# Kernel optimization log

Measured on AMD Instinct MI355X. Metric: run time of the kernel, lower is better.

## Reference

```python
import jax, jax.numpy as jnp
import numpy as np

B = 2_000_000
CLAMP_MIN = 0.01
NORM_EPS = 1e-5


def setup_inputs() -> dict:
    key = jax.random.key(0)
    F = jax.random.normal(key, (B, 3, 3), dtype=jnp.float32)
    # learned scalar parameters (per init_kwargs)
    youngs_modulus_log = jnp.asarray(13.0, dtype=jnp.float32)
    poissons_ratio = jnp.asarray(0.3, dtype=jnp.float32)
    yield_stress = jnp.asarray(3000.0, dtype=jnp.float32)
    return {
        "F": F,
        "youngs_modulus_log": youngs_modulus_log,
        "poissons_ratio": poissons_ratio,
        "yield_stress": yield_stress,
    }


def reference(F, youngs_modulus_log, poissons_ratio, yield_stress):
    # von-Mises return mapping on singular values of the deformation gradient
    youngs_modulus = jnp.exp(youngs_modulus_log)
    mu = youngs_modulus / (2.0 * (1.0 + poissons_ratio))  # shear modulus

    # batched 3x3 SVD: U (B,3,3), sigma (B,3), Vh (B,3,3)
    U, sigma, Vh = jnp.linalg.svd(F, full_matrices=False)

    sigma = jnp.maximum(sigma, CLAMP_MIN)
    epsilon = jnp.log(sigma)                                  # (B,3) Hencky strain
    epsilon_trace = jnp.sum(epsilon, axis=1, keepdims=True)   # (B,1)
    epsilon_bar = epsilon - epsilon_trace / 3.0               # deviatoric strain
    epsilon_bar_norm = jnp.linalg.norm(epsilon_bar, axis=1, keepdims=True) + NORM_EPS

    delta_gamma = epsilon_bar_norm - yield_stress / (2.0 * mu)  # (B,1)
    yield_epsilon = epsilon - (delta_gamma / epsilon_bar_norm) * epsilon_bar
    yield_sigma = jnp.exp(yield_epsilon)

    sigma = jnp.where(delta_gamma > 0.0, yield_sigma, sigma)  # (B,3)

    # F_corrected = U @ diag(sigma) @ Vh, fused without materializing diag
    F_corrected = jnp.einsum("bij,bj,bjk->bik", U, sigma, Vh)
    return F_corrected
```

## Files before the change

### kernel.cpp

```cpp
#include <hip/hip_runtime.h>
#include <math.h>

#define TPB 256
#define MPB (TPB * 2)

typedef float v2  __attribute__((ext_vector_type(2)));
typedef int   v2i __attribute__((ext_vector_type(2)));

static __device__ __forceinline__ v2 V2(float x){ v2 r; r.x = x; r.y = x; return r; }
static __device__ __forceinline__ v2 vfma(v2 a, v2 b, v2 c){ return __builtin_elementwise_fma(a, b, c); }
static __device__ __forceinline__ v2 vmax(v2 a, v2 b){ return __builtin_elementwise_max(a, b); }
static __device__ __forceinline__ v2 vabs(v2 a){ return __builtin_elementwise_abs(a); }
static __device__ __forceinline__ v2 vcps(v2 a, v2 b){ return __builtin_elementwise_copysign(a, b); }

static __device__ __forceinline__ v2 rsq2(v2 x){ v2 r; r.x = __builtin_amdgcn_rsqf(x.x);  r.y = __builtin_amdgcn_rsqf(x.y);  return r; }
static __device__ __forceinline__ v2 rcp2(v2 x){ v2 r; r.x = __builtin_amdgcn_rcpf(x.x);  r.y = __builtin_amdgcn_rcpf(x.y);  return r; }
static __device__ __forceinline__ v2 sqt2(v2 x){ v2 r; r.x = __builtin_amdgcn_sqrtf(x.x); r.y = __builtin_amdgcn_sqrtf(x.y); return r; }
static __device__ __forceinline__ v2 lg22(v2 x){ v2 r; r.x = __builtin_amdgcn_logf(x.x);  r.y = __builtin_amdgcn_logf(x.y);  return r; }
static __device__ __forceinline__ v2 ex22(v2 x){ v2 r; r.x = __builtin_amdgcn_exp2f(x.x); r.y = __builtin_amdgcn_exp2f(x.y); return r; }

static __device__ __forceinline__ v2 vsel(v2i m, v2 a, v2 b){
  v2i ai = __builtin_bit_cast(v2i, a), bi = __builtin_bit_cast(v2i, b);
  return __builtin_bit_cast(v2, (ai & m) | (bi & ~m));
}

__device__ __forceinline__ void jcs2(v2 app_in, v2 aqq_in, v2 apq,
                                     v2& c, v2& s,
                                     v2& app_out, v2& aqq_out)
{
  v2 d    = (aqq_in - app_in) * 0.5f;
  v2 r2   = vmax(vfma(d, d, apq * apq), V2(1e-60f));
  v2 invh = rsq2(r2);
  v2 h    = r2 * invh;
  v2 sg   = vcps(V2(1.0f), d);
  v2 ch   = h + vabs(d);
  v2 sh   = apq * sg;
  v2 w    = rsq2(vfma(ch, ch, sh * sh));
  c = ch * w;
  s = sh * w;
  v2 hs = h * sg;
  v2 m  = app_in + d;
  app_out = m - hs;
  aqq_out = m + hs;
}

__device__ __forceinline__ void jrot(v2& app, v2& aqq, v2& apq,
                                     v2& apk, v2& aqk,
                                     v2& vp0, v2& vp1, v2& vp2,
                                     v2& vq0, v2& vq1, v2& vq2)
{
  v2 c, s;
  jcs2(app, aqq, apq, c, s, app, aqq);
  apq = V2(0.0f);
  v2 pk = apk, qk = aqk;
  apk = c * pk - s * qk;
  aqk = s * pk + c * qk;
  v2 v;
  v = vp0; vp0 = c*v - s*vq0; vq0 = s*v + c*vq0;
  v = vp1; vp1 = c*v - s*vq1; vq1 = s*v + c*vq1;
  v = vp2; vp2 = c*v - s*vq2; vq2 = s*v + c*vq2;
}

#define CSWAP(li, lj, a0, a1, a2, b0, b1, b2)                                   \
  do {                                                                          \
    v2i _m = (li) < (lj);                                                       \
    v2 _t;                                                                      \
    _t = vsel(_m,(lj),(li)); (lj) = vsel(_m,(li),(lj)); (li) = _t;              \
    _t = vsel(_m,(b0),(a0)); (b0) = vsel(_m,(a0),(b0)); (a0) = _t;              \
    _t = vsel(_m,(b1),(a1)); (b1) = vsel(_m,(a1),(b1)); (a1) = _t;              \
    _t = vsel(_m,(b2),(a2)); (b2) = vsel(_m,(a2),(b2)); (a2) = _t;              \
  } while (0)

__global__ __launch_bounds__(TPB) void plastic_svd_kernel(
    const float* __restrict__ F,
    const float* __restrict__ p_yml,
    const float* __restrict__ p_nu,
    const float* __restrict__ p_ys,
    float* __restrict__ out,
    int nmat)
{
  __shared__ float lds[MPB * 9];
  const int tid = threadIdx.x;
  const int blockBase = blockIdx.x * MPB;
  const int gbase = blockBase * 9;
  const int rem = nmat - blockBase;
  const int nfl = (rem >= MPB ? MPB : rem) * 9;
  const int nfl4 = nfl >> 2;

  {
    const float4* g4 = (const float4*)(F + gbase);
    float4* l4 = (float4*)lds;
    #pragma unroll
    for (int k = 0; k < 5; ++k) {
      int i4 = k * TPB + tid;
      if (i4 < nfl4) l4[i4] = g4[i4];
    }
    int i = (nfl & ~3) + tid;
    if (i < nfl) lds[i] = F[gbase + i];
    for (int i2 = nfl + tid; i2 < MPB * 9; i2 += TPB) lds[i2] = 0.0f;
  }
  __syncthreads();

  const int mi0 = blockBase + tid;
  const int mi1 = blockBase + TPB + tid;
  const float* mA = &lds[tid * 9];
  const float* mB = &lds[(tid + TPB) * 9];
  v2 f00,f01,f02,f10,f11,f12,f20,f21,f22;
  f00.x=mA[0]; f01.x=mA[1]; f02.x=mA[2];
  f10.x=mA[3]; f11.x=mA[4]; f12.x=mA[5];
  f20.x=mA[6]; f21.x=mA[7]; f22.x=mA[8];
  f00.y=mB[0]; f01.y=mB[1]; f02.y=mB[2];
  f10.y=mB[3]; f11.y=mB[4]; f12.y=mB[5];
  f20.y=mB[6]; f21.y=mB[7]; f22.y=mB[8];

  const float mu_s = __builtin_amdgcn_exp2f(p_yml[0] * 1.44269504f) *
                     __builtin_amdgcn_rcpf(2.0f * (1.0f + p_nu[0]));
  const float qy_s = p_ys[0] * 0.5f * __builtin_amdgcn_rcpf(mu_s);
  const v2 qy = V2(qy_s);

  v2 s00 = f00*f00 + f10*f10 + f20*f20;
  v2 s11 = f01*f01 + f11*f11 + f21*f21;
  v2 s22 = f02*f02 + f12*f12 + f22*f22;
  v2 s01 = f00*f01 + f10*f11 + f20*f21;
  v2 s02 = f00*f02 + f10*f12 + f20*f22;
  v2 s12 = f01*f02 + f11*f12 + f21*f22;

  v2 v00,v01,v02,v10,v11,v12,v20,v21,v22;
  v2 c, s;

  jcs2(s00, s11, s01, c, s, s00, s11);
  { v2 pk = s02, qk = s12; s02 = c*pk - s*qk; s12 = s*pk + c*qk; }
  v00 = c;  v01 = s;
  v10 = -s; v11 = c;
  s01 = V2(0.0f);
  jcs2(s00, s22, s02, c, s, s00, s22);
  { v2 pk = s01, qk = s12; s01 = c*pk - s*qk; s12 = s*pk + c*qk; }
  v02 = s * v00; v12 = s * v10; v22 = c;
  v00 = c * v00; v10 = c * v10; v20 = -s;
  v21 = V2(0.0f);
  s02 = V2(0.0f);
  jrot(s11, s22, s12, s01, s02, v01, v11, v21, v02, v12, v22);
  jrot(s00, s11, s01, s02, s12, v00, v10, v20, v01, v11, v21);
  jrot(s00, s22, s02, s01, s12, v00, v10, v20, v02, v12, v22);
  jrot(s11, s22, s12, s01, s02, v01, v11, v21, v02, v12, v22);
  jrot(s00, s11, s01, s02, s12, v00, v10, v20, v01, v11, v21);
  jrot(s00, s22, s02, s01, s12, v00, v10, v20, v02, v12, v22);
  jcs2(s11, s22, s12, c, s, s11, s22);
  { v2 v;
    v = v01; v01 = c*v - s*v02; v02 = s*v + c*v02;
    v = v11; v11 = c*v - s*v12; v12 = s*v + c*v12;
    v = v21; v21 = c*v - s*v22; v22 = s*v + c*v22; }

  v2 l0 = s00, l1 = s11, l2 = s22;
  CSWAP(l0, l1, v00, v10, v20, v01, v11, v21);
  CSWAP(l1, l2, v01, v11, v21, v02, v12, v22);
  CSWAP(l0, l1, v00, v10, v20, v01, v11, v21);

  v2 w0x = f00*v00 + f01*v10 + f02*v20;
  v2 w0y = f10*v00 + f11*v10 + f12*v20;
  v2 w0z = f20*v00 + f21*v10 + f22*v20;
  v2 n0sq = w0x*w0x + w0y*w0y + w0z*w0z;
  v2 inv0 = rsq2(vmax(n0sq, V2(1e-40f)));
  v2 sig0 = n0sq * inv0;
  v2 u0x = w0x*inv0, u0y = w0y*inv0, u0z = w0z*inv0;

  v2 w1x = f00*v01 + f01*v11 + f02*v21;
  v2 w1y = f10*v01 + f11*v11 + f12*v21;
  v2 w1z = f20*v01 + f21*v11 + f22*v21;
  v2 sig1 = sqt2(w1x*w1x + w1y*w1y + w1z*w1z);
  v2 d01 = w1x*u0x + w1y*u0y + w1z*u0z;
  w1x = w1x - d01*u0x; w1y = w1y - d01*u0y; w1z = w1z - d01*u0z;
  v2 n1sq = w1x*w1x + w1y*w1y + w1z*w1z;
  v2 inv1 = rsq2(vmax(n1sq, V2(1e-40f)));
  v2 u1x = w1x*inv1, u1y = w1y*inv1, u1z = w1z*inv1;

  v2 u2x = u0y*u1z - u0z*u1y;
  v2 u2y = u0z*u1x - u0x*u1z;
  v2 u2z = u0x*u1y - u0y*u1x;
  v2 w2x = f00*v02 + f01*v12 + f02*v22;
  v2 w2y = f10*v02 + f11*v12 + f12*v22;
  v2 w2z = f20*v02 + f21*v12 + f22*v22;
  v2 s2d = u2x*w2x + u2y*w2y + u2z*w2z;
  v2i _neg = s2d < V2(0.0f);
  v2 sg = vsel(_neg, V2(-1.0f), V2(1.0f));
  v2 sig2 = s2d * sg;
  u2x = u2x * sg; u2y = u2y * sg; u2z = u2z * sg;

  v2 c0 = vmax(sig0, V2(0.01f));
  v2 c1 = vmax(sig1, V2(0.01f));
  v2 c2 = vmax(sig2, V2(0.01f));
  v2 e0 = lg22(c0), e1 = lg22(c1), e2 = lg22(c2);
  v2 m3 = (e0 + e1 + e2) * (1.0f / 3.0f);
  v2 b0 = e0 - m3, b1 = e1 - m3, b2 = e2 - m3;
  v2 bn = sqt2(b0*b0 + b1*b1 + b2*b2) * 0.69314718f + V2(1e-5f);
  v2 r = vmax(bn - qy, V2(0.0f)) * rcp2(bn);
  c0 = ex22(e0 - r * b0);
  c1 = ex22(e1 - r * b1);
  c2 = ex22(e2 - r * b2);

  v2 a0x = c0*u0x, a0y = c0*u0y, a0z = c0*u0z;
  v2 a1x = c1*u1x, a1y = c1*u1y, a1z = c1*u1z;
  v2 a2x = c2*u2x, a2y = c2*u2y, a2z = c2*u2z;

  v2 o00 = a0x*v00 + a1x*v01 + a2x*v02;
  v2 o01 = a0x*v10 + a1x*v11 + a2x*v12;
  v2 o02 = a0x*v20 + a1x*v21 + a2x*v22;
  v2 o10 = a0y*v00 + a1y*v01 + a2y*v02;
  v2 o11 = a0y*v10 + a1y*v11 + a2y*v12;
  v2 o12 = a0y*v20 + a1y*v21 + a2y*v22;
  v2 o20 = a0z*v00 + a1z*v01 + a2z*v02;
  v2 o21 = a0z*v10 + a1z*v11 + a2z*v12;
  v2 o22 = a0z*v20 + a1z*v21 + a2z*v22;

  if (mi0 < nmat) {
    float* m = &lds[tid * 9];
    m[0]=o00.x; m[1]=o01.x; m[2]=o02.x;
    m[3]=o10.x; m[4]=o11.x; m[5]=o12.x;
    m[6]=o20.x; m[7]=o21.x; m[8]=o22.x;
  }
  if (mi1 < nmat) {
    float* m = &lds[(tid + TPB) * 9];
    m[0]=o00.y; m[1]=o01.y; m[2]=o02.y;
    m[3]=o10.y; m[4]=o11.y; m[5]=o12.y;
    m[6]=o20.y; m[7]=o21.y; m[8]=o22.y;
  }
  __syncthreads();

  {
    float4* g4 = (float4*)(out + gbase);
    const float4* l4 = (const float4*)lds;
    #pragma unroll
    for (int k = 0; k < 5; ++k) {
      int i4 = k * TPB + tid;
      if (i4 < nfl4) g4[i4] = l4[i4];
    }
    int i = (nfl & ~3) + tid;
    if (i < nfl) out[gbase + i] = lds[i];
  }
}

extern "C" void kernel_launch(void* const* d_in, const int* in_sizes, int n_in,
                              void* d_out, int out_size, void* d_ws, size_t ws_size,
                              hipStream_t stream) {
  const float* F     = (const float*)d_in[0];
  const float* p_yml = (const float*)d_in[1];
  const float* p_nu  = (const float*)d_in[2];
  const float* p_ys  = (const float*)d_in[3];
  float* out = (float*)d_out;

  const int nmat = in_sizes[0] / 9;
  const int nblocks = (nmat + MPB - 1) / MPB;
  hipLaunchKernelGGL(plastic_svd_kernel, dim3(nblocks), dim3(TPB), 0, stream,
                     F, p_yml, p_nu, p_ys, out, nmat);
}
```

Before: 33.18 us.

## Process four matrices per thread with v4 vectors and reload F from LDS

```diff
diff --git a/kernel.cpp b/kernel.cpp
--- a/kernel.cpp
+++ b/kernel.cpp
@@ -2,60 +2,71 @@
 #include <math.h>
 
 #define TPB 256
-#define MPB (TPB * 2)
-
-typedef float v2  __attribute__((ext_vector_type(2)));
-typedef int   v2i __attribute__((ext_vector_type(2)));
-
-static __device__ __forceinline__ v2 V2(float x){ v2 r; r.x = x; r.y = x; return r; }
-static __device__ __forceinline__ v2 vfma(v2 a, v2 b, v2 c){ return __builtin_elementwise_fma(a, b, c); }
-static __device__ __forceinline__ v2 vmax(v2 a, v2 b){ return __builtin_elementwise_max(a, b); }
-static __device__ __forceinline__ v2 vabs(v2 a){ return __builtin_elementwise_abs(a); }
-static __device__ __forceinline__ v2 vcps(v2 a, v2 b){ return __builtin_elementwise_copysign(a, b); }
-
-static __device__ __forceinline__ v2 rsq2(v2 x){ v2 r; r.x = __builtin_amdgcn_rsqf(x.x);  r.y = __builtin_amdgcn_rsqf(x.y);  return r; }
-static __device__ __forceinline__ v2 rcp2(v2 x){ v2 r; r.x = __builtin_amdgcn_rcpf(x.x);  r.y = __builtin_amdgcn_rcpf(x.y);  return r; }
-static __device__ __forceinline__ v2 sqt2(v2 x){ v2 r; r.x = __builtin_amdgcn_sqrtf(x.x); r.y = __builtin_amdgcn_sqrtf(x.y); return r; }
-static __device__ __forceinline__ v2 lg22(v2 x){ v2 r; r.x = __builtin_amdgcn_logf(x.x);  r.y = __builtin_amdgcn_logf(x.y);  return r; }
-static __device__ __forceinline__ v2 ex22(v2 x){ v2 r; r.x = __builtin_amdgcn_exp2f(x.x); r.y = __builtin_amdgcn_exp2f(x.y); return r; }
-
-static __device__ __forceinline__ v2 vsel(v2i m, v2 a, v2 b){
-  v2i ai = __builtin_bit_cast(v2i, a), bi = __builtin_bit_cast(v2i, b);
-  return __builtin_bit_cast(v2, (ai & m) | (bi & ~m));
-}
-
-__device__ __forceinline__ void jcs2(v2 app_in, v2 aqq_in, v2 apq,
-                                     v2& c, v2& s,
-                                     v2& app_out, v2& aqq_out)
+#define NQ 4
+#define MPB (TPB * NQ)
+
+typedef float v4  __attribute__((ext_vector_type(4)));
+typedef int   v4i __attribute__((ext_vector_type(4)));
+
+static __device__ __forceinline__ v4 V4(float x){ v4 r; r.x=x; r.y=x; r.z=x; r.w=x; return r; }
+static __device__ __forceinline__ v4 vfma(v4 a, v4 b, v4 c){ return __builtin_elementwise_fma(a, b, c); }
+static __device__ __forceinline__ v4 vmax(v4 a, v4 b){ return __builtin_elementwise_max(a, b); }
+static __device__ __forceinline__ v4 vabs(v4 a){ return __builtin_elementwise_abs(a); }
+static __device__ __forceinline__ v4 vcps(v4 a, v4 b){ return __builtin_elementwise_copysign(a, b); }
+
+static __device__ __forceinline__ v4 rsq4(v4 x){
+  v4 r; r.x=__builtin_amdgcn_rsqf(x.x); r.y=__builtin_amdgcn_rsqf(x.y);
+        r.z=__builtin_amdgcn_rsqf(x.z); r.w=__builtin_amdgcn_rsqf(x.w); return r; }
+static __device__ __forceinline__ v4 rcp4(v4 x){
+  v4 r; r.x=__builtin_amdgcn_rcpf(x.x); r.y=__builtin_amdgcn_rcpf(x.y);
+        r.z=__builtin_amdgcn_rcpf(x.z); r.w=__builtin_amdgcn_rcpf(x.w); return r; }
+static __device__ __forceinline__ v4 sqt4(v4 x){
+  v4 r; r.x=__builtin_amdgcn_sqrtf(x.x); r.y=__builtin_amdgcn_sqrtf(x.y);
+        r.z=__builtin_amdgcn_sqrtf(x.z); r.w=__builtin_amdgcn_sqrtf(x.w); return r; }
+static __device__ __forceinline__ v4 lg24(v4 x){
+  v4 r; r.x=__builtin_amdgcn_logf(x.x); r.y=__builtin_amdgcn_logf(x.y);
+        r.z=__builtin_amdgcn_logf(x.z); r.w=__builtin_amdgcn_logf(x.w); return r; }
+static __device__ __forceinline__ v4 ex24(v4 x){
+  v4 r; r.x=__builtin_amdgcn_exp2f(x.x); r.y=__builtin_amdgcn_exp2f(x.y);
+        r.z=__builtin_amdgcn_exp2f(x.z); r.w=__builtin_amdgcn_exp2f(x.w); return r; }
+
+static __device__ __forceinline__ v4 vsel(v4i m, v4 a, v4 b){
+  v4i ai = __builtin_bit_cast(v4i, a), bi = __builtin_bit_cast(v4i, b);
+  return __builtin_bit_cast(v4, (ai & m) | (bi & ~m));
+}
+
+__device__ __forceinline__ void jcs2(v4 app_in, v4 aqq_in, v4 apq,
+                                     v4& c, v4& s,
+                                     v4& app_out, v4& aqq_out)
 {
-  v2 d    = (aqq_in - app_in) * 0.5f;
-  v2 r2   = vmax(vfma(d, d, apq * apq), V2(1e-60f));
-  v2 invh = rsq2(r2);
-  v2 h    = r2 * invh;
-  v2 sg   = vcps(V2(1.0f), d);
-  v2 ch   = h + vabs(d);
-  v2 sh   = apq * sg;
-  v2 w    = rsq2(vfma(ch, ch, sh * sh));
+  v4 d    = (aqq_in - app_in) * 0.5f;
+  v4 r2   = vmax(vfma(d, d, apq * apq), V4(1e-30f));
+  v4 invh = rsq4(r2);
+  v4 h    = r2 * invh;
+  v4 sg   = vcps(V4(1.0f), d);
+  v4 ch   = h + vabs(d);
+  v4 sh   = apq * sg;
+  v4 w    = rsq4(vfma(ch, ch, sh * sh));
   c = ch * w;
   s = sh * w;
-  v2 hs = h * sg;
-  v2 m  = app_in + d;
+  v4 hs = h * sg;
+  v4 m  = app_in + d;
   app_out = m - hs;
   aqq_out = m + hs;
 }
 
-__device__ __forceinline__ void jrot(v2& app, v2& aqq, v2& apq,
-                                     v2& apk, v2& aqk,
-                                     v2& vp0, v2& vp1, v2& vp2,
-                                     v2& vq0, v2& vq1, v2& vq2)
+__device__ __forceinline__ void jrot(v4& app, v4& aqq, v4& apq,
+                                     v4& apk, v4& aqk,
+                                     v4& vp0, v4& vp1, v4& vp2,
+                                     v4& vq0, v4& vq1, v4& vq2)
 {
-  v2 c, s;
+  v4 c, s;
   jcs2(app, aqq, apq, c, s, app, aqq);
-  apq = V2(0.0f);
-  v2 pk = apk, qk = aqk;
+  apq = V4(0.0f);
+  v4 pk = apk, qk = aqk;
   apk = c * pk - s * qk;
   aqk = s * pk + c * qk;
-  v2 v;
+  v4 v;
   v = vp0; vp0 = c*v - s*vq0; vq0 = s*v + c*vq0;
   v = vp1; vp1 = c*v - s*vq1; vq1 = s*v + c*vq1;
   v = vp2; vp2 = c*v - s*vq2; vq2 = s*v + c*vq2;
@@ -63,8 +74,8 @@
 
 #define CSWAP(li, lj, a0, a1, a2, b0, b1, b2)                                   \
   do {                                                                          \
-    v2i _m = (li) < (lj);                                                       \
-    v2 _t;                                                                      \
+    v4i _m = (li) < (lj);                                                       \
+    v4 _t;                                                                      \
     _t = vsel(_m,(lj),(li)); (lj) = vsel(_m,(li),(lj)); (li) = _t;              \
     _t = vsel(_m,(b0),(a0)); (b0) = vsel(_m,(a0),(b0)); (a0) = _t;              \
     _t = vsel(_m,(b1),(a1)); (b1) = vsel(_m,(a1),(b1)); (a1) = _t;              \
@@ -91,7 +102,7 @@
     const float4* g4 = (const float4*)(F + gbase);
     float4* l4 = (float4*)lds;
     #pragma unroll
-    for (int k = 0; k < 5; ++k) {
+    for (int k = 0; k < 9; ++k) {
       int i4 = k * TPB + tid;
       if (i4 < nfl4) l4[i4] = g4[i4];
     }
@@ -101,44 +112,44 @@
   }
   __syncthreads();
 
-  const int mi0 = blockBase + tid;
-  const int mi1 = blockBase + TPB + tid;
-  const float* mA = &lds[tid * 9];
-  const float* mB = &lds[(tid + TPB) * 9];
-  v2 f00,f01,f02,f10,f11,f12,f20,f21,f22;
-  f00.x=mA[0]; f01.x=mA[1]; f02.x=mA[2];
-  f10.x=mA[3]; f11.x=mA[4]; f12.x=mA[5];
-  f20.x=mA[6]; f21.x=mA[7]; f22.x=mA[8];
-  f00.y=mB[0]; f01.y=mB[1]; f02.y=mB[2];
-  f10.y=mB[3]; f11.y=mB[4]; f12.y=mB[5];
-  f20.y=mB[6]; f21.y=mB[7]; f22.y=mB[8];
+
+  v4 s00, s11, s22, s01, s02, s12;
+  {
+    v4 f00,f01,f02,f10,f11,f12,f20,f21,f22;
+    #pragma unroll
+    for (int q = 0; q < NQ; ++q) {
+      const float* m = &lds[(q * TPB + tid) * 9];
+      f00[q]=m[0]; f01[q]=m[1]; f02[q]=m[2];
+      f10[q]=m[3]; f11[q]=m[4]; f12[q]=m[5];
+      f20[q]=m[6]; f21[q]=m[7]; f22[q]=m[8];
+    }
+    s00 = f00*f00 + f10*f10 + f20*f20;
+    s11 = f01*f01 + f11*f11 + f21*f21;
+    s22 = f02*f02 + f12*f12 + f22*f22;
+    s01 = f00*f01 + f10*f11 + f20*f21;
+    s02 = f00*f02 + f10*f12 + f20*f22;
+    s12 = f01*f02 + f11*f12 + f21*f22;
+  }
 
   const float mu_s = __builtin_amdgcn_exp2f(p_yml[0] * 1.44269504f) *
                      __builtin_amdgcn_rcpf(2.0f * (1.0f + p_nu[0]));
   const float qy_s = p_ys[0] * 0.5f * __builtin_amdgcn_rcpf(mu_s);
-  const v2 qy = V2(qy_s);
-
-  v2 s00 = f00*f00 + f10*f10 + f20*f20;
-  v2 s11 = f01*f01 + f11*f11 + f21*f21;
-  v2 s22 = f02*f02 + f12*f12 + f22*f22;
-  v2 s01 = f00*f01 + f10*f11 + f20*f21;
-  v2 s02 = f00*f02 + f10*f12 + f20*f22;
-  v2 s12 = f01*f02 + f11*f12 + f21*f22;
-
-  v2 v00,v01,v02,v10,v11,v12,v20,v21,v22;
-  v2 c, s;
+  const v4 qy = V4(qy_s);
+
+  v4 v00,v01,v02,v10,v11,v12,v20,v21,v22;
+  v4 c, s;
 
   jcs2(s00, s11, s01, c, s, s00, s11);
-  { v2 pk = s02, qk = s12; s02 = c*pk - s*qk; s12 = s*pk + c*qk; }
+  { v4 pk = s02, qk = s12; s02 = c*pk - s*qk; s12 = s*pk + c*qk; }
   v00 = c;  v01 = s;
   v10 = -s; v11 = c;
-  s01 = V2(0.0f);
+  s01 = V4(0.0f);
   jcs2(s00, s22, s02, c, s, s00, s22);
-  { v2 pk = s01, qk = s12; s01 = c*pk - s*qk; s12 = s*pk + c*qk; }
+  { v4 pk = s01, qk = s12; s01 = c*pk - s*qk; s12 = s*pk + c*qk; }
   v02 = s * v00; v12 = s * v10; v22 = c;
   v00 = c * v00; v10 = c * v10; v20 = -s;
-  v21 = V2(0.0f);
-  s02 = V2(0.0f);
+  v21 = V4(0.0f);
+  s02 = V4(0.0f);
   jrot(s11, s22, s12, s01, s02, v01, v11, v21, v02, v12, v22);
   jrot(s00, s11, s01, s02, s12, v00, v10, v20, v01, v11, v21);
   jrot(s00, s22, s02, s01, s12, v00, v10, v20, v02, v12, v22);
@@ -146,83 +157,89 @@
   jrot(s00, s11, s01, s02, s12, v00, v10, v20, v01, v11, v21);
   jrot(s00, s22, s02, s01, s12, v00, v10, v20, v02, v12, v22);
   jcs2(s11, s22, s12, c, s, s11, s22);
-  { v2 v;
+  { v4 v;
     v = v01; v01 = c*v - s*v02; v02 = s*v + c*v02;
     v = v11; v11 = c*v - s*v12; v12 = s*v + c*v12;
     v = v21; v21 = c*v - s*v22; v22 = s*v + c*v22; }
 
-  v2 l0 = s00, l1 = s11, l2 = s22;
+  v4 l0 = s00, l1 = s11, l2 = s22;
   CSWAP(l0, l1, v00, v10, v20, v01, v11, v21);
   CSWAP(l1, l2, v01, v11, v21, v02, v12, v22);
   CSWAP(l0, l1, v00, v10, v20, v01, v11, v21);
 
-  v2 w0x = f00*v00 + f01*v10 + f02*v20;
-  v2 w0y = f10*v00 + f11*v10 + f12*v20;
-  v2 w0z = f20*v00 + f21*v10 + f22*v20;
-  v2 n0sq = w0x*w0x + w0y*w0y + w0z*w0z;
-  v2 inv0 = rsq2(vmax(n0sq, V2(1e-40f)));
-  v2 sig0 = n0sq * inv0;
-  v2 u0x = w0x*inv0, u0y = w0y*inv0, u0z = w0z*inv0;
-
-  v2 w1x = f00*v01 + f01*v11 + f02*v21;
-  v2 w1y = f10*v01 + f11*v11 + f12*v21;
-  v2 w1z = f20*v01 + f21*v11 + f22*v21;
-  v2 sig1 = sqt2(w1x*w1x + w1y*w1y + w1z*w1z);
-  v2 d01 = w1x*u0x + w1y*u0y + w1z*u0z;
+  v4 f00,f01,f02,f10,f11,f12,f20,f21,f22;
+  #pragma unroll
+  for (int q = 0; q < NQ; ++q) {
+    const float* m = &lds[(q * TPB + tid) * 9];
+    f00[q]=m[0]; f01[q]=m[1]; f02[q]=m[2];
+    f10[q]=m[3]; f11[q]=m[4]; f12[q]=m[5];
+    f20[q]=m[6]; f21[q]=m[7]; f22[q]=m[8];
+  }
+
+  v4 w0x = f00*v00 + f01*v10 + f02*v20;
+  v4 w0y = f10*v00 + f11*v10 + f12*v20;
+  v4 w0z = f20*v00 + f21*v10 + f22*v20;
+  v4 n0sq = w0x*w0x + w0y*w0y + w0z*w0z;
+  v4 inv0 = rsq4(vmax(n0sq, V4(1e-30f)));
+  v4 sig0 = n0sq * inv0;
+  v4 u0x = w0x*inv0, u0y = w0y*inv0, u0z = w0z*inv0;
+
+  v4 w1x = f00*v01 + f01*v11 + f02*v21;
+  v4 w1y = f10*v01 + f11*v11 + f12*v21;
+  v4 w1z = f20*v01 + f21*v11 + f22*v21;
+  v4 sig1 = sqt4(w1x*w1x + w1y*w1y + w1z*w1z);
+  v4 d01 = w1x*u0x + w1y*u0y + w1z*u0z;
   w1x = w1x - d01*u0x; w1y = w1y - d01*u0y; w1z = w1z - d01*u0z;
-  v2 n1sq = w1x*w1x + w1y*w1y + w1z*w1z;
-  v2 inv1 = rsq2(vmax(n1sq, V2(1e-40f)));
-  v2 u1x = w1x*inv1, u1y = w1y*inv1, u1z = w1z*inv1;
-
-  v2 u2x = u0y*u1z - u0z*u1y;
-  v2 u2y = u0z*u1x - u0x*u1z;
-  v2 u2z = u0x*u1y - u0y*u1x;
-  v2 w2x = f00*v02 + f01*v12 + f02*v22;
-  v2 w2y = f10*v02 + f11*v12 + f12*v22;
-  v2 w2z = f20*v02 + f21*v12 + f22*v22;
-  v2 s2d = u2x*w2x + u2y*w2y + u2z*w2z;
-  v2i _neg = s2d < V2(0.0f);
-  v2 sg = vsel(_neg, V2(-1.0f), V2(1.0f));
-  v2 sig2 = s2d * sg;
+  v4 n1sq = w1x*w1x + w1y*w1y + w1z*w1z;
+  v4 inv1 = rsq4(vmax(n1sq, V4(1e-30f)));
+  v4 u1x = w1x*inv1, u1y = w1y*inv1, u1z = w1z*inv1;
+
+  v4 u2x = u0y*u1z - u0z*u1y;
+  v4 u2y = u0z*u1x - u0x*u1z;
+  v4 u2z = u0x*u1y - u0y*u1x;
+  v4 w2x = f00*v02 + f01*v12 + f02*v22;
+  v4 w2y = f10*v02 + f11*v12 + f12*v22;
+  v4 w2z = f20*v02 + f21*v12 + f22*v22;
+  v4 s2d = u2x*w2x + u2y*w2y + u2z*w2z;
+  v4i _neg = s2d < V4(0.0f);
+  v4 sg = vsel(_neg, V4(-1.0f), V4(1.0f));
+  v4 sig2 = s2d * sg;
   u2x = u2x * sg; u2y = u2y * sg; u2z = u2z * sg;
 
-  v2 c0 = vmax(sig0, V2(0.01f));
-  v2 c1 = vmax(sig1, V2(0.01f));
-  v2 c2 = vmax(sig2, V2(0.01f));
-  v2 e0 = lg22(c0), e1 = lg22(c1), e2 = lg22(c2);
-  v2 m3 = (e0 + e1 + e2) * (1.0f / 3.0f);
-  v2 b0 = e0 - m3, b1 = e1 - m3, b2 = e2 - m3;
-  v2 bn = sqt2(b0*b0 + b1*b1 + b2*b2) * 0.69314718f + V2(1e-5f);
-  v2 r = vmax(bn - qy, V2(0.0f)) * rcp2(bn);
-  c0 = ex22(e0 - r * b0);
-  c1 = ex22(e1 - r * b1);
-  c2 = ex22(e2 - r * b2);
-
-  v2 a0x = c0*u0x, a0y = c0*u0y, a0z = c0*u0z;
-  v2 a1x = c1*u1x, a1y = c1*u1y, a1z = c1*u1z;
-  v2 a2x = c2*u2x, a2y = c2*u2y, a2z = c2*u2z;
-
-  v2 o00 = a0x*v00 + a1x*v01 + a2x*v02;
-  v2 o01 = a0x*v10 + a1x*v11 + a2x*v12;
-  v2 o02 = a0x*v20 + a1x*v21 + a2x*v22;
-  v2 o10 = a0y*v00 + a1y*v01 + a2y*v02;
-  v2 o11 = a0y*v10 + a1y*v11 + a2y*v12;
-  v2 o12 = a0y*v20 + a1y*v21 + a2y*v22;
-  v2 o20 = a0z*v00 + a1z*v01 + a2z*v02;
-  v2 o21 = a0z*v10 + a1z*v11 + a2z*v12;
-  v2 o22 = a0z*v20 + a1z*v21 + a2z*v22;
-
-  if (mi0 < nmat) {
-    float* m = &lds[tid * 9];
-    m[0]=o00.x; m[1]=o01.x; m[2]=o02.x;
-    m[3]=o10.x; m[4]=o11.x; m[5]=o12.x;
-    m[6]=o20.x; m[7]=o21.x; m[8]=o22.x;
-  }
-  if (mi1 < nmat) {
-    float* m = &lds[(tid + TPB) * 9];
-    m[0]=o00.y; m[1]=o01.y; m[2]=o02.y;
-    m[3]=o10.y; m[4]=o11.y; m[5]=o12.y;
-    m[6]=o20.y; m[7]=o21.y; m[8]=o22.y;
+  v4 c0 = vmax(sig0, V4(0.01f));
+  v4 c1 = vmax(sig1, V4(0.01f));
+  v4 c2 = vmax(sig2, V4(0.01f));
+  v4 e0 = lg24(c0), e1 = lg24(c1), e2 = lg24(c2);
+  v4 m3 = (e0 + e1 + e2) * (1.0f / 3.0f);
+  v4 b0 = e0 - m3, b1 = e1 - m3, b2 = e2 - m3;
+  v4 bn = sqt4(b0*b0 + b1*b1 + b2*b2) * 0.69314718f + V4(1e-5f);
+  v4 r = vmax(bn - qy, V4(0.0f)) * rcp4(bn);
+  c0 = ex24(e0 - r * b0);
+  c1 = ex24(e1 - r * b1);
+  c2 = ex24(e2 - r * b2);
+
+  v4 a0x = c0*u0x, a0y = c0*u0y, a0z = c0*u0z;
+  v4 a1x = c1*u1x, a1y = c1*u1y, a1z = c1*u1z;
+  v4 a2x = c2*u2x, a2y = c2*u2y, a2z = c2*u2z;
+
+  v4 o00 = a0x*v00 + a1x*v01 + a2x*v02;
+  v4 o01 = a0x*v10 + a1x*v11 + a2x*v12;
+  v4 o02 = a0x*v20 + a1x*v21 + a2x*v22;
+  v4 o10 = a0y*v00 + a1y*v01 + a2y*v02;
+  v4 o11 = a0y*v10 + a1y*v11 + a2y*v12;
+  v4 o12 = a0y*v20 + a1y*v21 + a2y*v22;
+  v4 o20 = a0z*v00 + a1z*v01 + a2z*v02;
+  v4 o21 = a0z*v10 + a1z*v11 + a2z*v12;
+  v4 o22 = a0z*v20 + a1z*v21 + a2z*v22;
+
+  #pragma unroll
+  for (int q = 0; q < NQ; ++q) {
+    if (blockBase + q * TPB + tid < nmat) {
+      float* m = &lds[(q * TPB + tid) * 9];
+      m[0]=o00[q]; m[1]=o01[q]; m[2]=o02[q];
+      m[3]=o10[q]; m[4]=o11[q]; m[5]=o12[q];
+      m[6]=o20[q]; m[7]=o21[q]; m[8]=o22[q];
+    }
   }
   __syncthreads();
 
@@ -230,7 +247,7 @@
     float4* g4 = (float4*)(out + gbase);
     const float4* l4 = (const float4*)lds;
     #pragma unroll
-    for (int k = 0; k < 5; ++k) {
+    for (int k = 0; k < 9; ++k) {
       int i4 = k * TPB + tid;
       if (i4 < nfl4) g4[i4] = l4[i4];
     }
```

New measurement: 36.47 us. 9.9% more time.

## Use persistent blocks with double-buffered async global-to-LDS loads and direct stores

Applied to the files above, without the earlier changes.

```diff
diff --git a/kernel.cpp b/kernel.cpp
--- a/kernel.cpp
+++ b/kernel.cpp
@@ -2,26 +2,36 @@
 #include <math.h>
 
 #define TPB 256
-#define MPB (TPB * 2)
+#define NQ 2
+#define CHUNK (TPB * NQ)
+#define CH_F (CHUNK * 9)
+#define CH_F4 (CH_F / 4)
 
 typedef float v2  __attribute__((ext_vector_type(2)));
 typedef int   v2i __attribute__((ext_vector_type(2)));
-
-static __device__ __forceinline__ v2 V2(float x){ v2 r; r.x = x; r.y = x; return r; }
+typedef float f4u __attribute__((ext_vector_type(4), aligned(4)));
+
+static __device__ __forceinline__ v2 V2(float x){ v2 r; r.x=x; r.y=x; return r; }
 static __device__ __forceinline__ v2 vfma(v2 a, v2 b, v2 c){ return __builtin_elementwise_fma(a, b, c); }
 static __device__ __forceinline__ v2 vmax(v2 a, v2 b){ return __builtin_elementwise_max(a, b); }
 static __device__ __forceinline__ v2 vabs(v2 a){ return __builtin_elementwise_abs(a); }
 static __device__ __forceinline__ v2 vcps(v2 a, v2 b){ return __builtin_elementwise_copysign(a, b); }
 
-static __device__ __forceinline__ v2 rsq2(v2 x){ v2 r; r.x = __builtin_amdgcn_rsqf(x.x);  r.y = __builtin_amdgcn_rsqf(x.y);  return r; }
-static __device__ __forceinline__ v2 rcp2(v2 x){ v2 r; r.x = __builtin_amdgcn_rcpf(x.x);  r.y = __builtin_amdgcn_rcpf(x.y);  return r; }
-static __device__ __forceinline__ v2 sqt2(v2 x){ v2 r; r.x = __builtin_amdgcn_sqrtf(x.x); r.y = __builtin_amdgcn_sqrtf(x.y); return r; }
-static __device__ __forceinline__ v2 lg22(v2 x){ v2 r; r.x = __builtin_amdgcn_logf(x.x);  r.y = __builtin_amdgcn_logf(x.y);  return r; }
-static __device__ __forceinline__ v2 ex22(v2 x){ v2 r; r.x = __builtin_amdgcn_exp2f(x.x); r.y = __builtin_amdgcn_exp2f(x.y); return r; }
+static __device__ __forceinline__ v2 rsq2(v2 x){ v2 r; r.x=__builtin_amdgcn_rsqf(x.x);  r.y=__builtin_amdgcn_rsqf(x.y);  return r; }
+static __device__ __forceinline__ v2 rcp2(v2 x){ v2 r; r.x=__builtin_amdgcn_rcpf(x.x);  r.y=__builtin_amdgcn_rcpf(x.y);  return r; }
+static __device__ __forceinline__ v2 sqt2(v2 x){ v2 r; r.x=__builtin_amdgcn_sqrtf(x.x); r.y=__builtin_amdgcn_sqrtf(x.y); return r; }
+static __device__ __forceinline__ v2 lg22(v2 x){ v2 r; r.x=__builtin_amdgcn_logf(x.x);  r.y=__builtin_amdgcn_logf(x.y);  return r; }
+static __device__ __forceinline__ v2 ex22(v2 x){ v2 r; r.x=__builtin_amdgcn_exp2f(x.x); r.y=__builtin_amdgcn_exp2f(x.y); return r; }
 
 static __device__ __forceinline__ v2 vsel(v2i m, v2 a, v2 b){
   v2i ai = __builtin_bit_cast(v2i, a), bi = __builtin_bit_cast(v2i, b);
-  return __builtin_bit_cast(v2, (ai & m) | (bi & ~m));
+  return __builtin_bit_cast(v2, bi ^ ((ai ^ bi) & m));
+}
+
+static __device__ __forceinline__ void gl_lds16(const float* g, float* l){
+  __builtin_amdgcn_global_load_lds(
+      (const __attribute__((address_space(1))) void*)g,
+      (__attribute__((address_space(3))) void*)l, 16, 0, 0);
 }
 
 __device__ __forceinline__ void jcs2(v2 app_in, v2 aqq_in, v2 apq,
@@ -29,7 +39,7 @@
                                      v2& app_out, v2& aqq_out)
 {
   v2 d    = (aqq_in - app_in) * 0.5f;
-  v2 r2   = vmax(vfma(d, d, apq * apq), V2(1e-60f));
+  v2 r2   = vmax(vfma(d, d, apq * apq), V2(1e-30f));
   v2 invh = rsq2(r2);
   v2 h    = r2 * invh;
   v2 sg   = vcps(V2(1.0f), d);
@@ -77,165 +87,177 @@
     const float* __restrict__ p_nu,
     const float* __restrict__ p_ys,
     float* __restrict__ out,
-    int nmat)
+    int nmat, int nchunks)
 {
-  __shared__ float lds[MPB * 9];
-  const int tid = threadIdx.x;
-  const int blockBase = blockIdx.x * MPB;
-  const int gbase = blockBase * 9;
-  const int rem = nmat - blockBase;
-  const int nfl = (rem >= MPB ? MPB : rem) * 9;
-  const int nfl4 = nfl >> 2;
-
-  {
-    const float4* g4 = (const float4*)(F + gbase);
-    float4* l4 = (float4*)lds;
-    #pragma unroll
-    for (int k = 0; k < 5; ++k) {
-      int i4 = k * TPB + tid;
-      if (i4 < nfl4) l4[i4] = g4[i4];
-    }
-    int i = (nfl & ~3) + tid;
-    if (i < nfl) lds[i] = F[gbase + i];
-    for (int i2 = nfl + tid; i2 < MPB * 9; i2 += TPB) lds[i2] = 0.0f;
-  }
-  __syncthreads();
-
-  const int mi0 = blockBase + tid;
-  const int mi1 = blockBase + TPB + tid;
-  const float* mA = &lds[tid * 9];
-  const float* mB = &lds[(tid + TPB) * 9];
-  v2 f00,f01,f02,f10,f11,f12,f20,f21,f22;
-  f00.x=mA[0]; f01.x=mA[1]; f02.x=mA[2];
-  f10.x=mA[3]; f11.x=mA[4]; f12.x=mA[5];
-  f20.x=mA[6]; f21.x=mA[7]; f22.x=mA[8];
-  f00.y=mB[0]; f01.y=mB[1]; f02.y=mB[2];
-  f10.y=mB[3]; f11.y=mB[4]; f12.y=mB[5];
-  f20.y=mB[6]; f21.y=mB[7]; f22.y=mB[8];
+  __shared__ float lds[2][CH_F];
+  const int tid  = threadIdx.x;
+  const int totF  = nmat * 9;
+  const int totF4 = totF >> 2;
 
   const float mu_s = __builtin_amdgcn_exp2f(p_yml[0] * 1.44269504f) *
                      __builtin_amdgcn_rcpf(2.0f * (1.0f + p_nu[0]));
   const float qy_s = p_ys[0] * 0.5f * __builtin_amdgcn_rcpf(mu_s);
   const v2 qy = V2(qy_s);
 
-  v2 s00 = f00*f00 + f10*f10 + f20*f20;
-  v2 s11 = f01*f01 + f11*f11 + f21*f21;
-  v2 s22 = f02*f02 + f12*f12 + f22*f22;
-  v2 s01 = f00*f01 + f10*f11 + f20*f21;
-  v2 s02 = f00*f02 + f10*f12 + f20*f22;
-  v2 s12 = f01*f02 + f11*f12 + f21*f22;
-
-  v2 v00,v01,v02,v10,v11,v12,v20,v21,v22;
-  v2 c, s;
-
-  jcs2(s00, s11, s01, c, s, s00, s11);
-  { v2 pk = s02, qk = s12; s02 = c*pk - s*qk; s12 = s*pk + c*qk; }
-  v00 = c;  v01 = s;
-  v10 = -s; v11 = c;
-  s01 = V2(0.0f);
-  jcs2(s00, s22, s02, c, s, s00, s22);
-  { v2 pk = s01, qk = s12; s01 = c*pk - s*qk; s12 = s*pk + c*qk; }
-  v02 = s * v00; v12 = s * v10; v22 = c;
-  v00 = c * v00; v10 = c * v10; v20 = -s;
-  v21 = V2(0.0f);
-  s02 = V2(0.0f);
-  jrot(s11, s22, s12, s01, s02, v01, v11, v21, v02, v12, v22);
-  jrot(s00, s11, s01, s02, s12, v00, v10, v20, v01, v11, v21);
-  jrot(s00, s22, s02, s01, s12, v00, v10, v20, v02, v12, v22);
-  jrot(s11, s22, s12, s01, s02, v01, v11, v21, v02, v12, v22);
-  jrot(s00, s11, s01, s02, s12, v00, v10, v20, v01, v11, v21);
-  jrot(s00, s22, s02, s01, s12, v00, v10, v20, v02, v12, v22);
-  jcs2(s11, s22, s12, c, s, s11, s22);
-  { v2 v;
-    v = v01; v01 = c*v - s*v02; v02 = s*v + c*v02;
-    v = v11; v11 = c*v - s*v12; v12 = s*v + c*v12;
-    v = v21; v21 = c*v - s*v22; v22 = s*v + c*v22; }
-
-  v2 l0 = s00, l1 = s11, l2 = s22;
-  CSWAP(l0, l1, v00, v10, v20, v01, v11, v21);
-  CSWAP(l1, l2, v01, v11, v21, v02, v12, v22);
-  CSWAP(l0, l1, v00, v10, v20, v01, v11, v21);
-
-  v2 w0x = f00*v00 + f01*v10 + f02*v20;
-  v2 w0y = f10*v00 + f11*v10 + f12*v20;
-  v2 w0z = f20*v00 + f21*v10 + f22*v20;
-  v2 n0sq = w0x*w0x + w0y*w0y + w0z*w0z;
-  v2 inv0 = rsq2(vmax(n0sq, V2(1e-40f)));
-  v2 sig0 = n0sq * inv0;
-  v2 u0x = w0x*inv0, u0y = w0y*inv0, u0z = w0z*inv0;
-
-  v2 w1x = f00*v01 + f01*v11 + f02*v21;
-  v2 w1y = f10*v01 + f11*v11 + f12*v21;
-  v2 w1z = f20*v01 + f21*v11 + f22*v21;
-  v2 sig1 = sqt2(w1x*w1x + w1y*w1y + w1z*w1z);
-  v2 d01 = w1x*u0x + w1y*u0y + w1z*u0z;
-  w1x = w1x - d01*u0x; w1y = w1y - d01*u0y; w1z = w1z - d01*u0z;
-  v2 n1sq = w1x*w1x + w1y*w1y + w1z*w1z;
-  v2 inv1 = rsq2(vmax(n1sq, V2(1e-40f)));
-  v2 u1x = w1x*inv1, u1y = w1y*inv1, u1z = w1z*inv1;
-
-  v2 u2x = u0y*u1z - u0z*u1y;
-  v2 u2y = u0z*u1x - u0x*u1z;
-  v2 u2z = u0x*u1y - u0y*u1x;
-  v2 w2x = f00*v02 + f01*v12 + f02*v22;
-  v2 w2y = f10*v02 + f11*v12 + f12*v22;
-  v2 w2z = f20*v02 + f21*v12 + f22*v22;
-  v2 s2d = u2x*w2x + u2y*w2y + u2z*w2z;
-  v2i _neg = s2d < V2(0.0f);
-  v2 sg = vsel(_neg, V2(-1.0f), V2(1.0f));
-  v2 sig2 = s2d * sg;
-  u2x = u2x * sg; u2y = u2y * sg; u2z = u2z * sg;
-
-  v2 c0 = vmax(sig0, V2(0.01f));
-  v2 c1 = vmax(sig1, V2(0.01f));
-  v2 c2 = vmax(sig2, V2(0.01f));
-  v2 e0 = lg22(c0), e1 = lg22(c1), e2 = lg22(c2);
-  v2 m3 = (e0 + e1 + e2) * (1.0f / 3.0f);
-  v2 b0 = e0 - m3, b1 = e1 - m3, b2 = e2 - m3;
-  v2 bn = sqt2(b0*b0 + b1*b1 + b2*b2) * 0.69314718f + V2(1e-5f);
-  v2 r = vmax(bn - qy, V2(0.0f)) * rcp2(bn);
-  c0 = ex22(e0 - r * b0);
-  c1 = ex22(e1 - r * b1);
-  c2 = ex22(e2 - r * b2);
-
-  v2 a0x = c0*u0x, a0y = c0*u0y, a0z = c0*u0z;
-  v2 a1x = c1*u1x, a1y = c1*u1y, a1z = c1*u1z;
-  v2 a2x = c2*u2x, a2y = c2*u2y, a2z = c2*u2z;
-
-  v2 o00 = a0x*v00 + a1x*v01 + a2x*v02;
-  v2 o01 = a0x*v10 + a1x*v11 + a2x*v12;
-  v2 o02 = a0x*v20 + a1x*v21 + a2x*v22;
-  v2 o10 = a0y*v00 + a1y*v01 + a2y*v02;
-  v2 o11 = a0y*v10 + a1y*v11 + a2y*v12;
-  v2 o12 = a0y*v20 + a1y*v21 + a2y*v22;
-  v2 o20 = a0z*v00 + a1z*v01 + a2z*v02;
-  v2 o21 = a0z*v10 + a1z*v11 + a2z*v12;
-  v2 o22 = a0z*v20 + a1z*v21 + a2z*v22;
-
-  if (mi0 < nmat) {
-    float* m = &lds[tid * 9];
-    m[0]=o00.x; m[1]=o01.x; m[2]=o02.x;
-    m[3]=o10.x; m[4]=o11.x; m[5]=o12.x;
-    m[6]=o20.x; m[7]=o21.x; m[8]=o22.x;
-  }
-  if (mi1 < nmat) {
-    float* m = &lds[(tid + TPB) * 9];
-    m[0]=o00.y; m[1]=o01.y; m[2]=o02.y;
-    m[3]=o10.y; m[4]=o11.y; m[5]=o12.y;
-    m[6]=o20.y; m[7]=o21.y; m[8]=o22.y;
-  }
-  __syncthreads();
-
-  {
-    float4* g4 = (float4*)(out + gbase);
-    const float4* l4 = (const float4*)lds;
+  auto STAGE = [&](int t, int b){
+    const int f4base = t * CH_F4;
     #pragma unroll
     for (int k = 0; k < 5; ++k) {
-      int i4 = k * TPB + tid;
-      if (i4 < nfl4) g4[i4] = l4[i4];
-    }
-    int i = (nfl & ~3) + tid;
-    if (i < nfl) out[gbase + i] = lds[i];
+      int i4  = k * TPB + tid;
+      int gi4 = f4base + i4;
+      if (i4 < CH_F4 && gi4 < totF4)
+        gl_lds16(F + gi4 * 4, &lds[b][i4 * 4]);
+    }
+    int e0 = totF4 << 2;
+    int e  = e0 + tid;
+    if (e < totF) {
+      int fb = t * CH_F;
+      if (e >= fb && e < fb + CH_F) lds[b][e - fb] = F[e];
+    }
+  };
+
+  int cur = 0;
+  STAGE(blockIdx.x, 0);
+  __syncthreads();
+
+  for (int t = blockIdx.x; t < nchunks; t += gridDim.x) {
+    int tn = t + gridDim.x;
+    if (tn < nchunks) STAGE(tn, cur ^ 1);
+
+    const int mbase = t * CHUNK;
+    const int mi0 = mbase + tid;
+    const int mi1 = mbase + TPB + tid;
+    const float* mA = &lds[cur][tid * 9];
+    const float* mB = &lds[cur][(TPB + tid) * 9];
+
+    v2 s00, s11, s22, s01, s02, s12;
+    {
+      v2 f00,f01,f02,f10,f11,f12,f20,f21,f22;
+      f00.x=mA[0]; f01.x=mA[1]; f02.x=mA[2];
+      f10.x=mA[3]; f11.x=mA[4]; f12.x=mA[5];
+      f20.x=mA[6]; f21.x=mA[7]; f22.x=mA[8];
+      f00.y=mB[0]; f01.y=mB[1]; f02.y=mB[2];
+      f10.y=mB[3]; f11.y=mB[4]; f12.y=mB[5];
+      f20.y=mB[6]; f21.y=mB[7]; f22.y=mB[8];
+      s00 = f00*f00 + f10*f10 + f20*f20;
+      s11 = f01*f01 + f11*f11 + f21*f21;
+      s22 = f02*f02 + f12*f12 + f22*f22;
+      s01 = f00*f01 + f10*f11 + f20*f21;
+      s02 = f00*f02 + f10*f12 + f20*f22;
+      s12 = f01*f02 + f11*f12 + f21*f22;
+    }
+
+    v2 v00,v01,v02,v10,v11,v12,v20,v21,v22;
+    v2 c, s;
+
+    jcs2(s00, s11, s01, c, s, s00, s11);
+    { v2 pk = s02, qk = s12; s02 = c*pk - s*qk; s12 = s*pk + c*qk; }
+    v00 = c;  v01 = s;
+    v10 = -s; v11 = c;
+    s01 = V2(0.0f);
+    jcs2(s00, s22, s02, c, s, s00, s22);
+    { v2 pk = s01, qk = s12; s01 = c*pk - s*qk; s12 = s*pk + c*qk; }
+    v02 = s * v00; v12 = s * v10; v22 = c;
+    v00 = c * v00; v10 = c * v10; v20 = -s;
+    v21 = V2(0.0f);
+    s02 = V2(0.0f);
+    jrot(s11, s22, s12, s01, s02, v01, v11, v21, v02, v12, v22);
+    jrot(s00, s11, s01, s02, s12, v00, v10, v20, v01, v11, v21);
+    jrot(s00, s22, s02, s01, s12, v00, v10, v20, v02, v12, v22);
+    jrot(s11, s22, s12, s01, s02, v01, v11, v21, v02, v12, v22);
+    jrot(s00, s11, s01, s02, s12, v00, v10, v20, v01, v11, v21);
+    jrot(s00, s22, s02, s01, s12, v00, v10, v20, v02, v12, v22);
+    jcs2(s11, s22, s12, c, s, s11, s22);
+    { v2 v;
+      v = v01; v01 = c*v - s*v02; v02 = s*v + c*v02;
+      v = v11; v11 = c*v - s*v12; v12 = s*v + c*v12;
+      v = v21; v21 = c*v - s*v22; v22 = s*v + c*v22; }
+
+    v2 l0 = s00, l1 = s11, l2 = s22;
+    CSWAP(l0, l1, v00, v10, v20, v01, v11, v21);
+    CSWAP(l1, l2, v01, v11, v21, v02, v12, v22);
+    CSWAP(l0, l1, v00, v10, v20, v01, v11, v21);
+
+    v2 f00,f01,f02,f10,f11,f12,f20,f21,f22;
+    f00.x=mA[0]; f01.x=mA[1]; f02.x=mA[2];
+    f10.x=mA[3]; f11.x=mA[4]; f12.x=mA[5];
+    f20.x=mA[6]; f21.x=mA[7]; f22.x=mA[8];
+    f00.y=mB[0]; f01.y=mB[1]; f02.y=mB[2];
+    f10.y=mB[3]; f11.y=mB[4]; f12.y=mB[5];
+    f20.y=mB[6]; f21.y=mB[7]; f22.y=mB[8];
+
+    v2 w0x = f00*v00 + f01*v10 + f02*v20;
+    v2 w0y = f10*v00 + f11*v10 + f12*v20;
+    v2 w0z = f20*v00 + f21*v10 + f22*v20;
+    v2 n0sq = w0x*w0x + w0y*w0y + w0z*w0z;
+    v2 inv0 = rsq2(vmax(n0sq, V2(1e-30f)));
+    v2 u0x = w0x*inv0, u0y = w0y*inv0, u0z = w0z*inv0;
+
+    v2 w1x = f00*v01 + f01*v11 + f02*v21;
+    v2 w1y = f10*v01 + f11*v11 + f12*v21;
+    v2 w1z = f20*v01 + f21*v11 + f22*v21;
+    v2 n1sq_pre = w1x*w1x + w1y*w1y + w1z*w1z;
+    v2 d01 = w1x*u0x + w1y*u0y + w1z*u0z;
+    w1x = w1x - d01*u0x; w1y = w1y - d01*u0y; w1z = w1z - d01*u0z;
+    v2 n1sq = w1x*w1x + w1y*w1y + w1z*w1z;
+    v2 inv1 = rsq2(vmax(n1sq, V2(1e-30f)));
+    v2 u1x = w1x*inv1, u1y = w1y*inv1, u1z = w1z*inv1;
+
+    v2 u2x = u0y*u1z - u0z*u1y;
+    v2 u2y = u0z*u1x - u0x*u1z;
+    v2 u2z = u0x*u1y - u0y*u1x;
+    v2 w2x = f00*v02 + f01*v12 + f02*v22;
+    v2 w2y = f10*v02 + f11*v12 + f12*v22;
+    v2 w2z = f20*v02 + f21*v12 + f22*v22;
+    v2 s2d = u2x*w2x + u2y*w2y + u2z*w2z;
+    v2 sg = vcps(V2(1.0f), s2d);
+    v2 sig2 = vabs(s2d);
+    u2x = u2x * sg; u2y = u2y * sg; u2z = u2z * sg;
+
+    v2 e0 = lg22(vmax(n0sq,     V2(1e-4f))) * 0.5f;
+    v2 e1 = lg22(vmax(n1sq_pre, V2(1e-4f))) * 0.5f;
+    v2 e2 = lg22(vmax(sig2,     V2(0.01f)));
+    v2 m3 = (e0 + e1 + e2) * (1.0f / 3.0f);
+    v2 b0 = e0 - m3, b1 = e1 - m3, b2 = e2 - m3;
+    v2 bn = sqt2(b0*b0 + b1*b1 + b2*b2) * 0.69314718f + V2(1e-5f);
+    v2 r = vmax(bn - qy, V2(0.0f)) * rcp2(bn);
+    v2 c0 = ex22(e0 - r * b0);
+    v2 c1 = ex22(e1 - r * b1);
+    v2 c2 = ex22(e2 - r * b2);
+
+    v2 a0x = c0*u0x, a0y = c0*u0y, a0z = c0*u0z;
+    v2 a1x = c1*u1x, a1y = c1*u1y, a1z = c1*u1z;
+    v2 a2x = c2*u2x, a2y = c2*u2y, a2z = c2*u2z;
+
+    v2 o00 = a0x*v00 + a1x*v01 + a2x*v02;
+    v2 o01 = a0x*v10 + a1x*v11 + a2x*v12;
+    v2 o02 = a0x*v20 + a1x*v21 + a2x*v22;
+    v2 o10 = a0y*v00 + a1y*v01 + a2y*v02;
+    v2 o11 = a0y*v10 + a1y*v11 + a2y*v12;
+    v2 o12 = a0y*v20 + a1y*v21 + a2y*v22;
+    v2 o20 = a0z*v00 + a1z*v01 + a2z*v02;
+    v2 o21 = a0z*v10 + a1z*v11 + a2z*v12;
+    v2 o22 = a0z*v20 + a1z*v21 + a2z*v22;
+
+    if (mi0 < nmat) {
+      float* p = out + mi0 * 9;
+      f4u a = {o00.x, o01.x, o02.x, o10.x};
+      f4u b = {o11.x, o12.x, o20.x, o21.x};
+      *(f4u*)(p)     = a;
+      *(f4u*)(p + 4) = b;
+      p[8] = o22.x;
+    }
+    if (mi1 < nmat) {
+      float* p = out + mi1 * 9;
+      f4u a = {o00.y, o01.y, o02.y, o10.y};
+      f4u b = {o11.y, o12.y, o20.y, o21.y};
+      *(f4u*)(p)     = a;
+      *(f4u*)(p + 4) = b;
+      p[8] = o22.y;
+    }
+
+    __syncthreads();
+    cur ^= 1;
   }
 }
 
@@ -249,7 +271,10 @@
   float* out = (float*)d_out;
 
   const int nmat = in_sizes[0] / 9;
-  const int nblocks = (nmat + MPB - 1) / MPB;
-  hipLaunchKernelGGL(plastic_svd_kernel, dim3(nblocks), dim3(TPB), 0, stream,
-                     F, p_yml, p_nu, p_ys, out, nmat);
-}
+  const int nchunks = (nmat + CHUNK - 1) / CHUNK;
+  int G = (nchunks + 3) / 4;
+  if (G > 1024) G = 1024;
+  if (G < 1) G = 1;
+  hipLaunchKernelGGL(plastic_svd_kernel, dim3(G), dim3(TPB), 0, stream,
+                     F, p_yml, p_nu, p_ys, out, nmat, nchunks);
+}
```

Result: slower. 38.53 us (+16.1%).
